# Optimization experiments

Hardware: AMD Instinct MI355X
Metric: run time of the kernel (lower is better)

Reference implementation:

```python
import jax, jax.numpy as jnp
import numpy as np

N = 50000
NFEAT, NHID, NCLASS, HEADS = 256, 64, 40, 4
HEAD_DIM = NHID // HEADS
E = 800000
NEG_SLOPE = 0.2


def _gat_conv(x, src, dst, W, a_src, a_dst, b, heads):
    # x: [N, F_in], W: [F_in, heads*C], a_src/a_dst: [heads, C], b: [heads*C]
    n = x.shape[0]
    h = (x @ W).reshape(n, heads, -1)                      # [N, H, C]
    alpha_s = jnp.einsum('nhc,hc->nh', h, a_src)           # [N, H]
    alpha_d = jnp.einsum('nhc,hc->nh', h, a_dst)
    e = jax.nn.leaky_relu(alpha_s[src] + alpha_d[dst], NEG_SLOPE)  # [E, H]
    # scatter-softmax over incoming edges per destination node
    e_max = jax.ops.segment_max(e, dst, num_segments=n)
    e_exp = jnp.exp(e - e_max[dst])
    denom = jax.ops.segment_sum(e_exp, dst, num_segments=n)
    alpha = e_exp / (denom[dst] + 1e-16)                   # [E, H]
    msg = h[src] * alpha[:, :, None]                       # [E, H, C]
    out = jax.ops.segment_sum(msg, dst, num_segments=n)    # [N, H, C]
    return out.reshape(n, -1) + b


def setup_inputs() -> dict:
    key = jax.random.key(0)
    ks = jax.random.split(key, 16)
    x = jax.random.normal(ks[0], (N, NFEAT), dtype=jnp.float32)
    edge_index = jax.random.randint(ks[1], (2, E), 0, N, dtype=jnp.int64)

    def glorot(k, shape):
        fan = sum(shape[:2]) if len(shape) > 1 else shape[0]
        return jax.random.normal(k, shape, dtype=jnp.float32) * (1.0 / np.sqrt(fan))

    inp = {'x': x, 'edge_index': edge_index}
    # conv1: nfeat -> heads*head_dim
    inp['W1'] = glorot(ks[2], (NFEAT, HEADS * HEAD_DIM))
    inp['a_src1'] = glorot(ks[3], (HEADS, HEAD_DIM))
    inp['a_dst1'] = glorot(ks[4], (HEADS, HEAD_DIM))
    inp['b1'] = jnp.zeros((HEADS * HEAD_DIM,), dtype=jnp.float32)
    # convx[0]: nhid -> heads*head_dim
    inp['W2'] = glorot(ks[5], (NHID, HEADS * HEAD_DIM))
    inp['a_src2'] = glorot(ks[6], (HEADS, HEAD_DIM))
    inp['a_dst2'] = glorot(ks[7], (HEADS, HEAD_DIM))
    inp['b2'] = jnp.zeros((HEADS * HEAD_DIM,), dtype=jnp.float32)
    # conv2: nhid -> nclass, heads=1
    inp['W3'] = glorot(ks[8], (NHID, NCLASS))
    inp['a_src3'] = glorot(ks[9], (1, NCLASS))
    inp['a_dst3'] = glorot(ks[10], (1, NCLASS))
    inp['b3'] = jnp.zeros((NCLASS,), dtype=jnp.float32)
    return inp


def reference(x, edge_index, W1, a_src1, a_dst1, b1, W2, a_src2, a_dst2, b2, W3, a_src3, a_dst3, b3):
    # add self-loops (PyG GATConv default add_self_loops=True)
    loop = jnp.arange(N, dtype=edge_index.dtype)
    src = jnp.concatenate([edge_index[0], loop])
    dst = jnp.concatenate([edge_index[1], loop])

    h = jax.nn.relu(_gat_conv(x, src, dst, W1, a_src1, a_dst1, b1, HEADS))
    h = jax.nn.relu(_gat_conv(h, src, dst, W2, a_src2, a_dst2, b2, HEADS))
    out = _gat_conv(h, src, dst, W3, a_src3, a_dst3, b3, 1)
    return out
```

## Files before the change

### kernel.cpp

```cpp
#include <hip/hip_runtime.h>

#define NEG_SLOPE 0.2f


__global__ void init_hist(int* __restrict__ hist, int n) {
    int i = blockIdx.x * blockDim.x + threadIdx.x;
    if (i < n) hist[i] = 1;
}

__global__ __launch_bounds__(256) void edge_hist(const int* __restrict__ ei,
                                                 int* __restrict__ hist,
                                                 int E, float inv8) {
    const int part = blockIdx.x & 7;
    const int base = (blockIdx.x >> 3) * 2048;
    const int end  = min(base + 2048, E);
    for (int i = base + (int)threadIdx.x; i < end; i += 256) {
        int d = ei[E + i];
        int pd = min((int)((float)d * inv8), 7);
        if (pd == part) atomicAdd(&hist[d], 1);
    }
}

__global__ __launch_bounds__(1024) void scan_kernel(const int* __restrict__ hist,
                                                    int* __restrict__ rowptr,
                                                    int* __restrict__ fill, int n) {
    __shared__ int wsum[16];
    __shared__ int carry_s;
    int tid = threadIdx.x;
    int lane = tid & 63, wid = tid >> 6;
    if (tid == 0) carry_s = 0;
    __syncthreads();
    for (int start = 0; start < n; start += 1024) {
        int i = start + tid;
        int v = (i < n) ? hist[i] : 0;
        int sv = v;
        #pragma unroll
        for (int d = 1; d < 64; d <<= 1) {
            int t = __shfl_up(sv, d);
            if (lane >= d) sv += t;
        }
        if (lane == 63) wsum[wid] = sv;
        __syncthreads();
        if (tid < 16) {
            int ws = wsum[tid];
            #pragma unroll
            for (int d = 1; d < 16; d <<= 1) {
                int t = __shfl_up(ws, d);
                if (tid >= d) ws += t;
            }
            wsum[tid] = ws;
        }
        __syncthreads();
        int base = carry_s;
        int waveoff = wid ? wsum[wid - 1] : 0;
        int excl = base + waveoff + sv - v;
        if (i < n) { rowptr[i] = excl; fill[i] = excl; }
        int tot = wsum[15];
        __syncthreads();
        if (tid == 0) carry_s = base + tot;
        __syncthreads();
    }
    if (tid == 0) rowptr[n] = carry_s;
}

__global__ __launch_bounds__(256) void scatter_part(const int* __restrict__ ei,
                                                    int* __restrict__ fill,
                                                    int* __restrict__ col,
                                                    int E, int M, float inv8) {
    const int part = blockIdx.x & 7;
    const int base = (blockIdx.x >> 3) * 2048;
    const int end  = min(base + 2048, M);
    for (int i = base + (int)threadIdx.x; i < end; i += 256) {
        int d = (i < E) ? ei[E + i] : (i - E);
        int pd = min((int)((float)d * inv8), 7);
        if (pd != part) continue;
        int s = (i < E) ? ei[i] : d;
        int pos = atomicAdd(&fill[d], 1);
        col[pos] = s;
    }
}


template <int K, int HC, int AH>
__global__ __launch_bounds__(256) void gemm_tiled(
    const float* __restrict__ x, const float* __restrict__ W,
    const float* __restrict__ a_src, const float* __restrict__ a_dst,
    float* __restrict__ h, float* __restrict__ as_, float* __restrict__ ad_,
    int n) {
    __shared__ float xs[64][68];
    __shared__ float ws[64][64];
    const int t = threadIdx.x;
    const int tx = t & 15;
    const int ty = t >> 4;
    const int rowBase = blockIdx.x * 64;

    float acc[4][4];
    #pragma unroll
    for (int r = 0; r < 4; ++r)
        #pragma unroll
        for (int c = 0; c < 4; ++c) acc[r][c] = 0.f;

    const int sr = t >> 2;
    const int sq = t & 3;

    #pragma unroll 1
    for (int kb = 0; kb < K; kb += 64) {
        __syncthreads();
        {
            int g = rowBase + sr;
            const float* xr = x + (size_t)g * K + kb;
            #pragma unroll
            for (int i = 0; i < 4; ++i) {
                int ko = sq * 16 + i * 4;
                float4 v = make_float4(0.f, 0.f, 0.f, 0.f);
                if (g < n) v = *(const float4*)(xr + ko);
                *(float4*)&xs[sr][ko] = v;
            }
        }
        if (HC == 64) {
            #pragma unroll
            for (int i = 0; i < 4; ++i) {
                int li = t + i * 256;
                int k = li >> 4, j4 = (li & 15) * 4;
                *(float4*)&ws[k][j4] = *(const float4*)&W[(size_t)(kb + k) * 64 + j4];
            }
        } else {
            for (int i = t; i < 64 * 64; i += 256) {
                int k = i >> 6, j = i & 63;
                ws[k][j] = (j < HC) ? W[(size_t)(kb + k) * HC + j] : 0.f;
            }
        }
        __syncthreads();

        #pragma unroll 2
        for (int k = 0; k < 64; k += 4) {
            float xr[4][4];
            #pragma unroll
            for (int r = 0; r < 4; ++r) {
                float4 v = *(const float4*)&xs[ty * 4 + r][k];
                xr[r][0] = v.x; xr[r][1] = v.y; xr[r][2] = v.z; xr[r][3] = v.w;
            }
            float wr[4][4];
            #pragma unroll
            for (int kk = 0; kk < 4; ++kk) {
                float4 v = *(const float4*)&ws[k + kk][tx * 4];
                wr[kk][0] = v.x; wr[kk][1] = v.y; wr[kk][2] = v.z; wr[kk][3] = v.w;
            }
            #pragma unroll
            for (int kk = 0; kk < 4; ++kk)
                #pragma unroll
                for (int r = 0; r < 4; ++r)
                    #pragma unroll
                    for (int c = 0; c < 4; ++c)
                        acc[r][c] = fmaf(xr[r][kk], wr[kk][c], acc[r][c]);
        }
    }

    if (AH == 4) {
        const int hh = tx >> 2;
        const int cb = (tx & 3) * 4;
        float asv[4], adv[4];
        #pragma unroll
        for (int c = 0; c < 4; ++c) {
            asv[c] = a_src[hh * 16 + cb + c];
            adv[c] = a_dst[hh * 16 + cb + c];
        }
        #pragma unroll
        for (int r = 0; r < 4; ++r) {
            float ps = 0.f, pd = 0.f;
            #pragma unroll
            for (int c = 0; c < 4; ++c) {
                ps = fmaf(acc[r][c], asv[c], ps);
                pd = fmaf(acc[r][c], adv[c], pd);
            }
            ps += __shfl_xor(ps, 1); ps += __shfl_xor(ps, 2);
            pd += __shfl_xor(pd, 1); pd += __shfl_xor(pd, 2);
            int g = rowBase + ty * 4 + r;
            if (g < n) {
                float4 v = make_float4(acc[r][0], acc[r][1], acc[r][2], acc[r][3]);
                *(float4*)&h[(size_t)g * 64 + tx * 4] = v;
                if ((tx & 3) == 0) {
                    as_[g * 4 + hh] = ps;
                    ad_[g * 4 + hh] = pd;
                }
            }
        }
    } else if (AH == 1) {
        const int cb = tx * 4;
        float asv[4], adv[4];
        #pragma unroll
        for (int c = 0; c < 4; ++c) {
            bool vld = (cb + c) < HC;
            asv[c] = vld ? a_src[cb + c] : 0.f;
            adv[c] = vld ? a_dst[cb + c] : 0.f;
        }
        #pragma unroll
        for (int r = 0; r < 4; ++r) {
            float ps = 0.f, pd = 0.f;
            #pragma unroll
            for (int c = 0; c < 4; ++c) {
                ps = fmaf(acc[r][c], asv[c], ps);
                pd = fmaf(acc[r][c], adv[c], pd);
            }
            ps += __shfl_xor(ps, 1); ps += __shfl_xor(ps, 2);
            ps += __shfl_xor(ps, 4); ps += __shfl_xor(ps, 8);
            pd += __shfl_xor(pd, 1); pd += __shfl_xor(pd, 2);
            pd += __shfl_xor(pd, 4); pd += __shfl_xor(pd, 8);
            int g = rowBase + ty * 4 + r;
            if (g < n) {
                if (tx * 4 < HC) {
                    float4 v = make_float4(acc[r][0], acc[r][1], acc[r][2], acc[r][3]);
                    *(float4*)&h[(size_t)g * HC + tx * 4] = v;
                }
                if (tx == 0) { as_[g] = ps; ad_[g] = pd; }
            }
        }
    } else {
        #pragma unroll
        for (int r = 0; r < 4; ++r) {
            int g = rowBase + ty * 4 + r;
            if (g < n && tx * 4 < HC) {
                float4 v = make_float4(acc[r][0], acc[r][1], acc[r][2], acc[r][3]);
                *(float4*)&h[(size_t)g * HC + tx * 4] = v;
            }
        }
    }
}

template <int H, int C, bool RELU>
__global__ __launch_bounds__(256) void aggr_kernel(
    const float* __restrict__ h, const float* __restrict__ as_,
    const float* __restrict__ ad_, const int* __restrict__ rowptr,
    const int* __restrict__ col, const float* __restrict__ b,
    float* __restrict__ out, int n) {
    constexpr int HC = H * C;
    __shared__ float wls[4][64][H];
    __shared__ int   sls[4][64];
    const int wib  = threadIdx.x >> 6;
    const int lane = threadIdx.x & 63;
    const int wid  = blockIdx.x * 4 + wib;
    if (wid >= n) return;

    const int p0 = rowptr[wid], p1 = rowptr[wid + 1];
    const int deg = p1 - p0;

    float adv[H];
    #pragma unroll
    for (int hh = 0; hh < H; ++hh) adv[hh] = ad_[wid * H + hh];

    const int myh = (HC < 64 && lane >= HC) ? 0 : lane / C;

    float m[H], sum[H];
    #pragma unroll
    for (int hh = 0; hh < H; ++hh) { m[hh] = -3.4e38f; sum[hh] = 0.f; }
    float acc = 0.f;

    for (int ch = 0; ch * 64 < deg; ++ch) {
        const int idx = p0 + ch * 64 + lane;
        const bool valid = idx < p1;
        int s = 0;
        float e[H];
        if (valid) {
            s = col[idx];
            if (H == 4) {
                float4 a4 = *(const float4*)&as_[s * 4];
                e[0] = a4.x + adv[0]; e[1] = a4.y + adv[1];
                e[2] = a4.z + adv[2]; e[3] = a4.w + adv[3];
            } else {
                e[0] = as_[s] + adv[0];
            }
            #pragma unroll
            for (int hh = 0; hh < H; ++hh)
                e[hh] = (e[hh] >= 0.f) ? e[hh] : NEG_SLOPE * e[hh];
        } else {
            #pragma unroll
            for (int hh = 0; hh < H; ++hh) e[hh] = -3.4e38f;
        }
        float f[H], w[H];
        #pragma unroll
        for (int hh = 0; hh < H; ++hh) {
            float v = e[hh];
            #pragma unroll
            for (int d = 1; d < 64; d <<= 1) v = fmaxf(v, __shfl_xor(v, d));
            float mn = fmaxf(m[hh], v);
            f[hh] = expf(m[hh] - mn);
            m[hh] = mn;
            w[hh] = expf(e[hh] - mn);
        }
        #pragma unroll
        for (int hh = 0; hh < H; ++hh) {
            float v = w[hh];
            #pragma unroll
            for (int d = 1; d < 64; d <<= 1) v += __shfl_xor(v, d);
            sum[hh] = sum[hh] * f[hh] + v;
        }
        #pragma unroll
        for (int hh = 0; hh < H; ++hh) wls[wib][lane][hh] = w[hh];
        sls[wib][lane] = s;
        __builtin_amdgcn_wave_barrier();

        float fmy;
        if (H == 1) fmy = f[0];
        else {
            float a = (myh & 1) ? f[1] : f[0];
            float c2 = (myh & 1) ? f[3] : f[2];
            fmy = (myh & 2) ? c2 : a;
        }
        acc *= fmy;

        const int cnt = min(64, deg - ch * 64);
        int p = 0;
        for (; p + 4 <= cnt; p += 4) {
            int s0 = sls[wib][p],     s1 = sls[wib][p + 1];
            int s2 = sls[wib][p + 2], s3 = sls[wib][p + 3];
            float w0 = wls[wib][p][myh],     w1 = wls[wib][p + 1][myh];
            float w2 = wls[wib][p + 2][myh], w3 = wls[wib][p + 3][myh];
            float h0 = 0.f, h1 = 0.f, h2 = 0.f, h3 = 0.f;
            if (lane < HC) {
                h0 = h[(size_t)s0 * HC + lane];
                h1 = h[(size_t)s1 * HC + lane];
                h2 = h[(size_t)s2 * HC + lane];
                h3 = h[(size_t)s3 * HC + lane];
            }
            acc = fmaf(w0, h0, acc);
            acc = fmaf(w1, h1, acc);
            acc = fmaf(w2, h2, acc);
            acc = fmaf(w3, h3, acc);
        }
        for (; p < cnt; ++p) {
            int ss = sls[wib][p];
            float ww = wls[wib][p][myh];
            float hv = (lane < HC) ? h[(size_t)ss * HC + lane] : 0.f;
            acc = fmaf(ww, hv, acc);
        }
        __builtin_amdgcn_wave_barrier();
    }

    if (lane < HC) {
        float smy;
        if (H == 1) smy = sum[0];
        else {
            float a = (myh & 1) ? sum[1] : sum[0];
            float c2 = (myh & 1) ? sum[3] : sum[2];
            smy = (myh & 2) ? c2 : a;
        }
        float r = acc / (smy + 1e-16f) + b[lane];
        out[(size_t)wid * HC + lane] = RELU ? fmaxf(r, 0.f) : r;
    }
}


extern "C" void kernel_launch(void* const* d_in, const int* in_sizes, int n_in,
                              void* d_out, int out_size, void* d_ws, size_t ws_size,
                              hipStream_t stream) {
    const float* x      = (const float*)d_in[0];
    const int*   ei     = (const int*)d_in[1];
    const float* W1     = (const float*)d_in[2];
    const float* a_src1 = (const float*)d_in[3];
    const float* a_dst1 = (const float*)d_in[4];
    const float* b1     = (const float*)d_in[5];
    const float* W2     = (const float*)d_in[6];
    const float* a_src2 = (const float*)d_in[7];
    const float* a_dst2 = (const float*)d_in[8];
    const float* b2     = (const float*)d_in[9];
    const float* W3     = (const float*)d_in[10];
    const float* a_src3 = (const float*)d_in[11];
    const float* a_dst3 = (const float*)d_in[12];
    const float* b3     = (const float*)d_in[13];
    float* out = (float*)d_out;

    const int NFEAT = 256, NHID = 64;
    const int N = in_sizes[0] / NFEAT;
    const int E = in_sizes[1] / 2;
    const int M = E + N;
    const float inv8 = 8.0f / (float)N;

    char* p = (char*)d_ws;
    auto alloc = [&](size_t bytes) {
        char* r = p;
        p += (bytes + 255) & ~(size_t)255;
        return r;
    };
    int*   hist   = (int*)alloc((size_t)N * 4);
    int*   rowptr = (int*)alloc((size_t)(N + 1) * 4);
    int*   fill   = (int*)alloc((size_t)N * 4);
    int*   col    = (int*)alloc((size_t)M * 4);
    float* hbuf   = (float*)alloc((size_t)N * NHID * 4);
    float* xbuf   = (float*)alloc((size_t)N * NHID * 4);
    float* asb    = (float*)alloc((size_t)N * 4 * 4);
    float* adb    = (float*)alloc((size_t)N * 4 * 4);

    dim3 blk(256);
    const int gemmGrid = (N + 63) / 64;
    const int aggrGrid = (N + 3) / 4;

    init_hist<<<(N + 255) / 256, blk, 0, stream>>>(hist, N);
    edge_hist<<<8 * ((E + 2047) / 2048), blk, 0, stream>>>(ei, hist, E, inv8);
    scan_kernel<<<1, 1024, 0, stream>>>(hist, rowptr, fill, N);
    scatter_part<<<8 * ((M + 2047) / 2048), blk, 0, stream>>>(ei, fill, col, E, M, inv8);

    gemm_tiled<256, 64, 4><<<gemmGrid, blk, 0, stream>>>(
        x, W1, a_src1, a_dst1, hbuf, asb, adb, N);
    aggr_kernel<4, 16, true><<<aggrGrid, blk, 0, stream>>>(
        hbuf, asb, adb, rowptr, col, b1, xbuf, N);

    gemm_tiled<64, 64, 4><<<gemmGrid, blk, 0, stream>>>(
        xbuf, W2, a_src2, a_dst2, hbuf, asb, adb, N);
    aggr_kernel<4, 16, true><<<aggrGrid, blk, 0, stream>>>(
        hbuf, asb, adb, rowptr, col, b2, xbuf, N);

    gemm_tiled<64, 40, 1><<<gemmGrid, blk, 0, stream>>>(
        xbuf, W3, a_src3, a_dst3, hbuf, asb, adb, N);
    aggr_kernel<1, 40, false><<<aggrGrid, blk, 0, stream>>>(
        hbuf, asb, adb, rowptr, col, b3, out, N);
}
```

Measured before the change: 411.8 us.

## Replace single-block prefix scan with three-pass multi-block scan

The CSR row-pointer scan previously ran in one 1024-thread block that looped serially over all 50k nodes with several barriers per chunk. It is now split into a per-chunk reduction kernel, a tiny single-wave scan of the block sums, and a final per-chunk scan that writes rowptr and fill. This spreads the scan across about 25 blocks, at the cost of two extra kernel launches and the hard limit that there can be at most 64 chunks (N up to 131072).

New measurement: 374.2 us. 1.1x faster.

```diff
diff --git a/kernel.cpp b/kernel.cpp
--- a/kernel.cpp
+++ b/kernel.cpp
@@ -1,6 +1,7 @@
 #include <hip/hip_runtime.h>
 
 #define NEG_SLOPE 0.2f
+#define SCAN_CHUNK 2048
 
 
 __global__ void init_hist(int* __restrict__ hist, int n) {
@@ -21,46 +22,72 @@
     }
 }
 
-__global__ __launch_bounds__(1024) void scan_kernel(const int* __restrict__ hist,
-                                                    int* __restrict__ rowptr,
-                                                    int* __restrict__ fill, int n) {
-    __shared__ int wsum[16];
-    __shared__ int carry_s;
-    int tid = threadIdx.x;
-    int lane = tid & 63, wid = tid >> 6;
-    if (tid == 0) carry_s = 0;
+
+__global__ __launch_bounds__(256) void scan_partial(const int* __restrict__ hist,
+                                                    int* __restrict__ bsum, int n) {
+    const int base = blockIdx.x * SCAN_CHUNK;
+    const int tid = threadIdx.x;
+    int s = 0;
+    #pragma unroll
+    for (int i = 0; i < 8; ++i) {
+        int idx = base + tid * 8 + i;
+        if (idx < n) s += hist[idx];
+    }
+    #pragma unroll
+    for (int d = 1; d < 64; d <<= 1) s += __shfl_xor(s, d);
+    __shared__ int wsum[4];
+    if ((tid & 63) == 0) wsum[tid >> 6] = s;
     __syncthreads();
-    for (int start = 0; start < n; start += 1024) {
-        int i = start + tid;
-        int v = (i < n) ? hist[i] : 0;
-        int sv = v;
-        #pragma unroll
-        for (int d = 1; d < 64; d <<= 1) {
-            int t = __shfl_up(sv, d);
-            if (lane >= d) sv += t;
-        }
-        if (lane == 63) wsum[wid] = sv;
-        __syncthreads();
-        if (tid < 16) {
-            int ws = wsum[tid];
-            #pragma unroll
-            for (int d = 1; d < 16; d <<= 1) {
-                int t = __shfl_up(ws, d);
-                if (tid >= d) ws += t;
-            }
-            wsum[tid] = ws;
-        }
-        __syncthreads();
-        int base = carry_s;
-        int waveoff = wid ? wsum[wid - 1] : 0;
-        int excl = base + waveoff + sv - v;
-        if (i < n) { rowptr[i] = excl; fill[i] = excl; }
-        int tot = wsum[15];
-        __syncthreads();
-        if (tid == 0) carry_s = base + tot;
-        __syncthreads();
-    }
-    if (tid == 0) rowptr[n] = carry_s;
+    if (tid == 0) bsum[blockIdx.x] = wsum[0] + wsum[1] + wsum[2] + wsum[3];
+}
+
+__global__ void scan_bsums(const int* __restrict__ bsum, int* __restrict__ boff,
+                           int nb, int* __restrict__ rowptr, int n) {
+    const int tid = threadIdx.x;
+    int v = (tid < nb) ? bsum[tid] : 0;
+    int sv = v;
+    #pragma unroll
+    for (int d = 1; d < 64; d <<= 1) {
+        int t = __shfl_up(sv, d);
+        if (tid >= d) sv += t;
+    }
+    if (tid < nb) boff[tid] = sv - v;
+    if (tid == 63) rowptr[n] = sv;
+}
+
+__global__ __launch_bounds__(256) void scan_final(const int* __restrict__ hist,
+                                                  const int* __restrict__ boff,
+                                                  int* __restrict__ rowptr,
+                                                  int* __restrict__ fill, int n) {
+    const int base = blockIdx.x * SCAN_CHUNK;
+    const int tid = threadIdx.x;
+    const int lane = tid & 63, wv = tid >> 6;
+    int vals[8];
+    int s = 0;
+    #pragma unroll
+    for (int i = 0; i < 8; ++i) {
+        int idx = base + tid * 8 + i;
+        vals[i] = (idx < n) ? hist[idx] : 0;
+        s += vals[i];
+    }
+    int sv = s;
+    #pragma unroll
+    for (int d = 1; d < 64; d <<= 1) {
+        int t = __shfl_up(sv, d);
+        if (lane >= d) sv += t;
+    }
+    __shared__ int wsum[4];
+    if (lane == 63) wsum[wv] = sv;
+    __syncthreads();
+    int woff = 0;
+    for (int i = 0; i < wv; ++i) woff += wsum[i];
+    int excl = boff[blockIdx.x] + woff + sv - s;
+    #pragma unroll
+    for (int i = 0; i < 8; ++i) {
+        int idx = base + tid * 8 + i;
+        if (idx < n) { rowptr[idx] = excl; fill[idx] = excl; }
+        excl += vals[i];
+    }
 }
 
 __global__ __launch_bounds__(256) void scatter_part(const int* __restrict__ ei,
@@ -374,6 +401,7 @@
     const int E = in_sizes[1] / 2;
     const int M = E + N;
     const float inv8 = 8.0f / (float)N;
+    const int nb = (N + SCAN_CHUNK - 1) / SCAN_CHUNK;
 
     char* p = (char*)d_ws;
     auto alloc = [&](size_t bytes) {
@@ -389,6 +417,8 @@
     float* xbuf   = (float*)alloc((size_t)N * NHID * 4);
     float* asb    = (float*)alloc((size_t)N * 4 * 4);
     float* adb    = (float*)alloc((size_t)N * 4 * 4);
+    int*   bsum   = (int*)alloc((size_t)64 * 4);
+    int*   boff   = (int*)alloc((size_t)64 * 4);
 
     dim3 blk(256);
     const int gemmGrid = (N + 63) / 64;
@@ -396,7 +426,9 @@
 
     init_hist<<<(N + 255) / 256, blk, 0, stream>>>(hist, N);
     edge_hist<<<8 * ((E + 2047) / 2048), blk, 0, stream>>>(ei, hist, E, inv8);
-    scan_kernel<<<1, 1024, 0, stream>>>(hist, rowptr, fill, N);
+    scan_partial<<<nb, blk, 0, stream>>>(hist, bsum, N);
+    scan_bsums<<<1, 64, 0, stream>>>(bsum, boff, nb, rowptr, N);
+    scan_final<<<nb, blk, 0, stream>>>(hist, boff, rowptr, fill, N);
     scatter_part<<<8 * ((M + 2047) / 2048), blk, 0, stream>>>(ei, fill, col, E, M, inv8);
 
     gemm_tiled<256, 64, 4><<<gemmGrid, blk, 0, stream>>>(
```
